# Optimization experiments

Hardware: AMD Instinct MI355X
Metric: run time of the kernel (lower is better)

The kernel has to match this reference:

```python
import jax, jax.numpy as jnp
import numpy as np

N_NODES = 100000
N_EDGES = 1600000
FEATURE_DIM, CONDITION_DIM, HIDDEN_DIM, LATENT_DIM = 256, 64, 128, 64


def setup_inputs() -> dict:
    key = jax.random.key(0)
    ks = jax.random.split(key, 12)

    def glorot(k, fan_in, fan_out):
        s = np.sqrt(6.0 / (fan_in + fan_out)).astype(np.float32)
        return jax.random.uniform(k, (fan_in, fan_out), jnp.float32, -s, s)

    return {
        "feature": jax.random.normal(ks[0], (N_NODES, FEATURE_DIM), jnp.float32),
        "condition": jax.random.normal(ks[1], (N_NODES, CONDITION_DIM), jnp.float32),
        "edge_index": jax.random.randint(ks[2], (2, N_EDGES), 0, N_NODES, jnp.int64),
        "W_f2h": glorot(ks[3], FEATURE_DIM, HIDDEN_DIM),
        "b_f2h": jnp.zeros((HIDDEN_DIM,), jnp.float32),
        "W_c2h": glorot(ks[4], CONDITION_DIM, HIDDEN_DIM),
        "b_c2h": jnp.zeros((HIDDEN_DIM,), jnp.float32),
        "W_h2h": glorot(ks[5], 2 * HIDDEN_DIM, HIDDEN_DIM),
        "b_h2h": jnp.zeros((HIDDEN_DIM,), jnp.float32),
        "W_h2l": glorot(ks[6], HIDDEN_DIM, LATENT_DIM),
        "b_h2l": jnp.zeros((LATENT_DIM,), jnp.float32),
    }


def reference(feature, condition, edge_index, W_f2h, b_f2h, W_c2h, b_c2h,
              W_h2h, b_h2h, W_h2l, b_h2l):
    N = feature.shape[0]
    self_loops = jnp.arange(N, dtype=edge_index.dtype)
    src = jnp.concatenate([edge_index[0], self_loops])  # message sources (j)
    dst = jnp.concatenate([edge_index[1], self_loops])  # message targets (i)

    # symmetric GCN normalization: D^{-1/2} (A+I) D^{-1/2}
    deg = jax.ops.segment_sum(jnp.ones(dst.shape[0], feature.dtype), dst,
                              num_segments=N)
    dinv = jnp.where(deg > 0, jax.lax.rsqrt(deg), 0.0)
    norm = dinv[src] * dinv[dst]  # [E+N]

    def gcn_conv(x, W, b):
        xl = x @ W                                   # [N, out]
        msg = xl[src] * norm[:, None]                # gather + scale
        return jax.ops.segment_sum(msg, dst, num_segments=N) + b

    f2h = jnp.tanh(gcn_conv(feature, W_f2h, b_f2h))
    c2h = jnp.tanh(gcn_conv(condition, W_c2h, b_c2h))
    h = jnp.concatenate([f2h, c2h], axis=1)          # [N, 2*hidden]
    h = jnp.tanh(gcn_conv(h, W_h2h, b_h2h))
    z = gcn_conv(h, W_h2l, b_h2l)
    return z
```

## Files before the change

kernel.cpp:

```cpp
#include <hip/hip_runtime.h>
#include <cmath>
#include <cstdint>


typedef _Float16 f16;
typedef _Float16 f16x8 __attribute__((ext_vector_type(8)));
typedef float f32x4 __attribute__((ext_vector_type(4)));
typedef unsigned int u32x4 __attribute__((ext_vector_type(4)));

__global__ void count_zero_kernel(int* __restrict__ count, int N) {
    int i = blockIdx.x * 256 + threadIdx.x;
    if (i < N) count[i] = 0;
}

__global__ void count_rank_kernel(const int* __restrict__ dst, int* __restrict__ count,
                                  int* __restrict__ rank, int E) {
    int e = blockIdx.x * 256 + threadIdx.x;
    if (e < E) rank[e] = atomicAdd(&count[dst[e]], 1);
}

__global__ void dinv_kernel(const int* __restrict__ count, float* __restrict__ dinv, int N) {
    int i = blockIdx.x * 256 + threadIdx.x;
    if (i < N) dinv[i] = rsqrtf((float)(count[i] + 1));
}

constexpr int SCAN_VPT = 8;
constexpr int SCAN_TILE = 256 * SCAN_VPT;

__global__ __launch_bounds__(256) void scan_partial_kernel(const int* __restrict__ count,
                                                           int* __restrict__ blocksums, int N) {
    __shared__ int red[256];
    const int t = threadIdx.x;
    int base = blockIdx.x * SCAN_TILE + t * SCAN_VPT;
    int s = 0;
#pragma unroll
    for (int i = 0; i < SCAN_VPT; ++i) {
        int idx = base + i;
        if (idx < N) s += count[idx];
    }
    red[t] = s;
    __syncthreads();
    for (int off = 128; off > 0; off >>= 1) {
        if (t < off) red[t] += red[t + off];
        __syncthreads();
    }
    if (t == 0) blocksums[blockIdx.x] = red[0];
}

__global__ __launch_bounds__(1024) void scan_blocksums_kernel(int* __restrict__ blocksums, int nb) {
    __shared__ int sh[1024];
    const int t = threadIdx.x;
    int v = (t < nb) ? blocksums[t] : 0;
    sh[t] = v;
    __syncthreads();
    for (int off = 1; off < 1024; off <<= 1) {
        int u = (t >= off) ? sh[t - off] : 0;
        __syncthreads();
        sh[t] += u;
        __syncthreads();
    }
    if (t < nb) blocksums[t] = sh[t] - v;
}

__global__ __launch_bounds__(256) void scan_final_kernel(const int* __restrict__ count,
                                                         const int* __restrict__ blocksums,
                                                         int* __restrict__ row_ptr, int N) {
    __shared__ int red[256];
    const int t = threadIdx.x;
    int base = blockIdx.x * SCAN_TILE + t * SCAN_VPT;
    int vals[SCAN_VPT];
    int s = 0;
#pragma unroll
    for (int i = 0; i < SCAN_VPT; ++i) {
        int idx = base + i;
        vals[i] = (idx < N) ? count[idx] : 0;
        s += vals[i];
    }
    red[t] = s;
    __syncthreads();
    for (int off = 1; off < 256; off <<= 1) {
        int u = (t >= off) ? red[t - off] : 0;
        __syncthreads();
        red[t] += u;
        __syncthreads();
    }
    int run = red[t] - s + blocksums[blockIdx.x];
#pragma unroll
    for (int i = 0; i < SCAN_VPT; ++i) {
        int idx = base + i;
        if (idx < N) {
            row_ptr[idx] = run;
            run += vals[i];
            if (idx == N - 1) row_ptr[N] = run;
        }
    }
}

__global__ void fill_kernel(const int* __restrict__ src, const int* __restrict__ dst,
                            const int* __restrict__ rank, const float* __restrict__ dinv,
                            const int* __restrict__ row_ptr, long long* __restrict__ csr, int E) {
    int e = blockIdx.x * 256 + threadIdx.x;
    if (e >= E) return;
    int s = src[e];
    int d = dst[e];
    int pos = row_ptr[d] + rank[e];
    float nrm = dinv[s] * dinv[d];
    long long v = ((long long)(unsigned)__float_as_int(nrm) << 32) | (unsigned)s;
    __builtin_nontemporal_store(v, csr + pos);
}

__global__ void wprep_kernel(const float* __restrict__ W, f16* __restrict__ wt_hi,
                             f16* __restrict__ wt_lo, int K, int M) {
    int idx = blockIdx.x * 256 + threadIdx.x;
    if (idx >= K * M) return;
    int k = idx / M, m = idx % M;
    float w = W[idx];
    f16 h = (f16)w;
    wt_hi[(size_t)m * K + k] = h;
    wt_lo[(size_t)m * K + k] = (f16)(w - (float)h);
}

__global__ void f32to16_kernel(const float* __restrict__ x, f16* __restrict__ y, int n4) {
    int i = blockIdx.x * 256 + threadIdx.x;
    if (i < n4) {
        float4 v = ((const float4*)x)[i];
        union { f16 h[4]; uint2 u; } p;
        p.h[0] = (f16)v.x; p.h[1] = (f16)v.y; p.h[2] = (f16)v.z; p.h[3] = (f16)v.w;
        ((uint2*)y)[i] = p.u;
    }
}

template <int K, int M, bool BIAS_TANH, bool X_IS_HALF>
__global__ __launch_bounds__(256) void gemm_mfma_kernel(
    const void* __restrict__ Xv, const f16* __restrict__ Wth,
    const f16* __restrict__ Wtl, const float* __restrict__ bias,
    f16* __restrict__ out, int ld, int colOff, int N) {
    constexpr int BM = 128, BK = 32, XP = 40;
    constexpr int SW = M / 4;
    constexpr int CT = SW / 16;
    constexpr int RT = BM / 16;
    __shared__ f16 xs[BM * XP];
    __shared__ f16 whs[M * XP];
    __shared__ f16 wls[M * XP];

    const int tid = threadIdx.x;
    const int lane = tid & 63;
    const int wv = tid >> 6;
    const int m16 = lane & 15;
    const int quad = lane >> 4;
    const int row0 = blockIdx.x * BM;

    f32x4 acc[RT][CT];
#pragma unroll
    for (int rt = 0; rt < RT; ++rt)
#pragma unroll
        for (int ct = 0; ct < CT; ++ct) acc[rt][ct] = (f32x4){0.f, 0.f, 0.f, 0.f};

    for (int k0 = 0; k0 < K; k0 += BK) {
        if (X_IS_HALF) {
            const f16* X = (const f16*)Xv;
#pragma unroll
            for (int i = 0; i < 2; ++i) {
                int c = i * 256 + tid;
                int r = c >> 2, ko = (c & 3) * 8;
                uint4 v = make_uint4(0u, 0u, 0u, 0u);
                if (row0 + r < N) v = *(const uint4*)(X + (size_t)(row0 + r) * K + k0 + ko);
                *(uint4*)(&xs[r * XP + ko]) = v;
            }
        } else {
            const float* X = (const float*)Xv;
#pragma unroll
            for (int i = 0; i < 4; ++i) {
                int c = i * 256 + tid;
                int r = c >> 3, kq = (c & 7) * 4;
                float4 v = make_float4(0.f, 0.f, 0.f, 0.f);
                if (row0 + r < N) v = *(const float4*)(X + (size_t)(row0 + r) * K + k0 + kq);
                union { f16 h[4]; uint2 u; } p;
                p.h[0] = (f16)v.x; p.h[1] = (f16)v.y; p.h[2] = (f16)v.z; p.h[3] = (f16)v.w;
                *(uint2*)(&xs[r * XP + kq]) = p.u;
            }
        }
#pragma unroll
        for (int i = 0; i < (M * 4) / 256; ++i) {
            int c = i * 256 + tid;
            int n = c >> 2, ko = (c & 3) * 8;
            *(uint4*)(&whs[n * XP + ko]) = *(const uint4*)(Wth + (size_t)n * K + k0 + ko);
            *(uint4*)(&wls[n * XP + ko]) = *(const uint4*)(Wtl + (size_t)n * K + k0 + ko);
        }
        __syncthreads();

        f16x8 bh[CT], bl[CT];
#pragma unroll
        for (int ct = 0; ct < CT; ++ct) {
            bh[ct] = *(const f16x8*)(&whs[(wv * SW + ct * 16 + m16) * XP + quad * 8]);
            bl[ct] = *(const f16x8*)(&wls[(wv * SW + ct * 16 + m16) * XP + quad * 8]);
        }
#pragma unroll
        for (int rt = 0; rt < RT; ++rt) {
            f16x8 a = *(const f16x8*)(&xs[(rt * 16 + m16) * XP + quad * 8]);
#pragma unroll
            for (int ct = 0; ct < CT; ++ct) {
                acc[rt][ct] = __builtin_amdgcn_mfma_f32_16x16x32_f16(a, bh[ct], acc[rt][ct], 0, 0, 0);
                acc[rt][ct] = __builtin_amdgcn_mfma_f32_16x16x32_f16(a, bl[ct], acc[rt][ct], 0, 0, 0);
            }
        }
        __syncthreads();
    }

    float brs[CT];
    if (BIAS_TANH) {
#pragma unroll
        for (int ct = 0; ct < CT; ++ct) brs[ct] = bias[wv * SW + ct * 16 + m16];
    }

#pragma unroll
    for (int rt = 0; rt < RT; ++rt) {
#pragma unroll
        for (int r = 0; r < 4; ++r) {
            int row = row0 + rt * 16 + quad * 4 + r;
            if (row < N) {
                f16* op = out + (size_t)row * ld + colOff + wv * SW + m16;
#pragma unroll
                for (int ct = 0; ct < CT; ++ct) {
                    float v = acc[rt][ct][r];
                    if (BIAS_TANH) v = tanhf(v + brs[ct]);
                    op[ct * 16] = (f16)v;
                }
            }
        }
    }
}

template <int M, bool TANH, bool HAS_BIAS, bool OUT_F32>
__global__ __launch_bounds__(256) void gather_h_kernel(
    const f16* __restrict__ xl, const float* __restrict__ b,
    const float* __restrict__ dinv, const int* __restrict__ row_ptr,
    const int2* __restrict__ csr, void* __restrict__ outv,
    int ld, int colOff, int N) {
    constexpr int TPN = M / 8;
    int gid = blockIdx.x * 256 + threadIdx.x;
    int node = gid / TPN;
    int t = gid % TPN;
    if (node >= N) return;

    float di = dinv[node];
    float self = di * di;
    f16x8 x = *(const f16x8*)(xl + (size_t)node * M + t * 8);
    float acc[8];
#pragma unroll
    for (int j = 0; j < 8; ++j) acc[j] = (float)x[j] * self;
    if (HAS_BIAS) {
        float4 b0 = *(const float4*)(b + t * 8);
        float4 b1 = *(const float4*)(b + t * 8 + 4);
        acc[0] += b0.x; acc[1] += b0.y; acc[2] += b0.z; acc[3] += b0.w;
        acc[4] += b1.x; acc[5] += b1.y; acc[6] += b1.z; acc[7] += b1.w;
    }

    int p = row_ptr[node];
    const int p1 = row_ptr[node + 1];
    for (; p + 4 <= p1; p += 4) {
        int2 e0 = csr[p];
        int2 e1 = csr[p + 1];
        int2 e2 = csr[p + 2];
        int2 e3 = csr[p + 3];
        f16x8 v0 = *(const f16x8*)(xl + (size_t)e0.x * M + t * 8);
        f16x8 v1 = *(const f16x8*)(xl + (size_t)e1.x * M + t * 8);
        f16x8 v2 = *(const f16x8*)(xl + (size_t)e2.x * M + t * 8);
        f16x8 v3 = *(const f16x8*)(xl + (size_t)e3.x * M + t * 8);
        float n0 = __int_as_float(e0.y);
        float n1 = __int_as_float(e1.y);
        float n2 = __int_as_float(e2.y);
        float n3 = __int_as_float(e3.y);
#pragma unroll
        for (int j = 0; j < 8; ++j)
            acc[j] += ((float)v0[j] * n0 + (float)v1[j] * n1) +
                      ((float)v2[j] * n2 + (float)v3[j] * n3);
    }
    for (; p < p1; ++p) {
        int2 e0 = csr[p];
        f16x8 v0 = *(const f16x8*)(xl + (size_t)e0.x * M + t * 8);
        float n0 = __int_as_float(e0.y);
#pragma unroll
        for (int j = 0; j < 8; ++j) acc[j] += (float)v0[j] * n0;
    }

    if (TANH) {
#pragma unroll
        for (int j = 0; j < 8; ++j) acc[j] = tanhf(acc[j]);
    }

    if (OUT_F32) {
        float* op = (float*)outv + (size_t)node * ld + colOff + t * 8;
        f32x4 o0 = {acc[0], acc[1], acc[2], acc[3]};
        f32x4 o1 = {acc[4], acc[5], acc[6], acc[7]};
        __builtin_nontemporal_store(o0, (f32x4*)op);
        __builtin_nontemporal_store(o1, (f32x4*)(op + 4));
    } else {
        union { f16 h[8]; u32x4 u; } o;
#pragma unroll
        for (int j = 0; j < 8; ++j) o.h[j] = (f16)acc[j];
        __builtin_nontemporal_store(o.u, (u32x4*)((f16*)outv + (size_t)node * ld + colOff + t * 8));
    }
}

extern "C" void kernel_launch(void* const* d_in, const int* in_sizes, int n_in,
                              void* d_out, int out_size, void* d_ws, size_t ws_size,
                              hipStream_t stream) {
    const int FD = 256;

    const float* feature   = (const float*)d_in[0];
    const float* condition = (const float*)d_in[1];
    const int*   edge      = (const int*)d_in[2];
    const float* W_f2h = (const float*)d_in[3];
    const float* b_f2h = (const float*)d_in[4];
    const float* W_c2h = (const float*)d_in[5];
    const float* b_c2h = (const float*)d_in[6];
    const float* W_h2h = (const float*)d_in[7];
    const float* b_h2h = (const float*)d_in[8];
    const float* W_h2l = (const float*)d_in[9];
    const float* b_h2l = (const float*)d_in[10];
    float* out = (float*)d_out;

    const int N = in_sizes[0] / FD;
    const int E = in_sizes[2] / 2;
    const int* src = edge;
    const int* dst = edge + E;

    float* ws_f   = (float*)d_ws;
    float* dinv   = ws_f;
    int*   count  = (int*)(ws_f + N);
    int*   rowp   = count + N;
    int*   bsums  = rowp + N + 1;
    int*   rank   = bsums + 1024;
    long long* csr = (long long*)(((uintptr_t)(rank + E) + 15) & ~(uintptr_t)15);
    f16*   A_h    = (f16*)(csr + E);
    f16*   B_h    = A_h + (size_t)N * 128;
    f16*   cond_h = B_h + (size_t)N * 256;
    f16*   wt1h   = cond_h + (size_t)N * 64;
    f16*   wt1l   = wt1h + 128 * 256;
    f16*   wt2h   = wt1l + 128 * 256;
    f16*   wt2l   = wt2h + 128 * 64;
    f16*   wt3h   = wt2l + 128 * 64;
    f16*   wt3l   = wt3h + 128 * 256;
    f16*   wt4h   = wt3l + 128 * 256;
    f16*   wt4l   = wt4h + 64 * 128;

    const int TB = 256;
    dim3 blk(TB);
    const int nScanBlocks = (N + SCAN_TILE - 1) / SCAN_TILE;

    wprep_kernel<<<(256 * 128 + TB - 1) / TB, blk, 0, stream>>>(W_f2h, wt1h, wt1l, 256, 128);
    wprep_kernel<<<(64 * 128 + TB - 1) / TB, blk, 0, stream>>>(W_c2h, wt2h, wt2l, 64, 128);
    wprep_kernel<<<(256 * 128 + TB - 1) / TB, blk, 0, stream>>>(W_h2h, wt3h, wt3l, 256, 128);
    wprep_kernel<<<(128 * 64 + TB - 1) / TB, blk, 0, stream>>>(W_h2l, wt4h, wt4l, 128, 64);
    f32to16_kernel<<<(N * 16 + TB - 1) / TB, blk, 0, stream>>>(condition, cond_h, N * 16);

    count_zero_kernel<<<(N + TB - 1) / TB, blk, 0, stream>>>(count, N);
    count_rank_kernel<<<(E + TB - 1) / TB, blk, 0, stream>>>(dst, count, rank, E);
    dinv_kernel<<<(N + TB - 1) / TB, blk, 0, stream>>>(count, dinv, N);
    scan_partial_kernel<<<nScanBlocks, blk, 0, stream>>>(count, bsums, N);
    scan_blocksums_kernel<<<1, 1024, 0, stream>>>(bsums, nScanBlocks);
    scan_final_kernel<<<nScanBlocks, blk, 0, stream>>>(count, bsums, rowp, N);
    fill_kernel<<<(E + TB - 1) / TB, blk, 0, stream>>>(src, dst, rank, dinv, rowp, csr, E);

    const int gemm_grid = (N + 127) / 128;
    const int g128 = (N * 16 + TB - 1) / TB;
    const int g64  = (N * 8 + TB - 1) / TB;

    gemm_mfma_kernel<256, 128, false, false><<<gemm_grid, blk, 0, stream>>>(
        feature, wt1h, wt1l, nullptr, A_h, 128, 0, N);
    gather_h_kernel<128, true, true, false><<<g128, blk, 0, stream>>>(
        A_h, b_f2h, dinv, rowp, (const int2*)csr, B_h, 256, 0, N);

    gather_h_kernel<64, false, false, false><<<g64, blk, 0, stream>>>(
        cond_h, nullptr, dinv, rowp, (const int2*)csr, A_h, 64, 0, N);
    gemm_mfma_kernel<64, 128, true, true><<<gemm_grid, blk, 0, stream>>>(
        A_h, wt2h, wt2l, b_c2h, B_h, 256, 128, N);

    gemm_mfma_kernel<256, 128, false, true><<<gemm_grid, blk, 0, stream>>>(
        B_h, wt3h, wt3l, nullptr, A_h, 128, 0, N);
    gather_h_kernel<128, true, true, false><<<g128, blk, 0, stream>>>(
        A_h, b_h2h, dinv, rowp, (const int2*)csr, B_h, 128, 0, N);

    gemm_mfma_kernel<128, 64, false, true><<<gemm_grid, blk, 0, stream>>>(
        B_h, wt4h, wt4l, nullptr, A_h, 64, 0, N);
    gather_h_kernel<64, false, true, true><<<g64, blk, 0, stream>>>(
        A_h, b_h2l, dinv, rowp, (const int2*)csr, out, 64, 0, N);
}
```

Baseline: 738.1 us.

## Fuse feature and condition gathers over interleaved XL buffer; prefetch CSR edges

The first GEMM output and the fp16 condition are written side by side in one 192-wide row buffer, so a single fused gather kernel aggregates both over the graph in one CSR pass. This removes a separate gather launch and a second read of the CSR structure. The gather loops now software-prefetch the next four CSR entries with nontemporal loads and handle the tail by masking instead of a scalar remainder loop. The cost is wider strided rows per gathered node, partly padded loads in the masked tail, and an extra ldx parameter on the GEMM.

```diff
diff --git a/kernel.cpp b/kernel.cpp
--- a/kernel.cpp
+++ b/kernel.cpp
@@ -5,8 +5,10 @@
 
 typedef _Float16 f16;
 typedef _Float16 f16x8 __attribute__((ext_vector_type(8)));
+typedef _Float16 f16x4 __attribute__((ext_vector_type(4)));
 typedef float f32x4 __attribute__((ext_vector_type(4)));
 typedef unsigned int u32x4 __attribute__((ext_vector_type(4)));
+typedef unsigned int u32x2 __attribute__((ext_vector_type(2)));
 
 __global__ void count_zero_kernel(int* __restrict__ count, int N) {
     int i = blockIdx.x * 256 + threadIdx.x;
@@ -120,21 +122,21 @@
     wt_lo[(size_t)m * K + k] = (f16)(w - (float)h);
 }
 
-__global__ void f32to16_kernel(const float* __restrict__ x, f16* __restrict__ y, int n4) {
+__global__ void cond_to_xl_kernel(const float* __restrict__ x, f16* __restrict__ XL, int N) {
     int i = blockIdx.x * 256 + threadIdx.x;
-    if (i < n4) {
-        float4 v = ((const float4*)x)[i];
-        union { f16 h[4]; uint2 u; } p;
-        p.h[0] = (f16)v.x; p.h[1] = (f16)v.y; p.h[2] = (f16)v.z; p.h[3] = (f16)v.w;
-        ((uint2*)y)[i] = p.u;
-    }
+    if (i >= N * 16) return;
+    int node = i >> 4, q = i & 15;
+    float4 v = ((const float4*)x)[i];
+    union { f16 h[4]; uint2 u; } p;
+    p.h[0] = (f16)v.x; p.h[1] = (f16)v.y; p.h[2] = (f16)v.z; p.h[3] = (f16)v.w;
+    *(uint2*)(XL + (size_t)node * 192 + 128 + q * 4) = p.u;
 }
 
 template <int K, int M, bool BIAS_TANH, bool X_IS_HALF>
 __global__ __launch_bounds__(256) void gemm_mfma_kernel(
     const void* __restrict__ Xv, const f16* __restrict__ Wth,
     const f16* __restrict__ Wtl, const float* __restrict__ bias,
-    f16* __restrict__ out, int ld, int colOff, int N) {
+    f16* __restrict__ out, int ld, int colOff, int ldx, int N) {
     constexpr int BM = 128, BK = 32, XP = 40;
     constexpr int SW = M / 4;
     constexpr int CT = SW / 16;
@@ -164,7 +166,7 @@
                 int c = i * 256 + tid;
                 int r = c >> 2, ko = (c & 3) * 8;
                 uint4 v = make_uint4(0u, 0u, 0u, 0u);
-                if (row0 + r < N) v = *(const uint4*)(X + (size_t)(row0 + r) * K + k0 + ko);
+                if (row0 + r < N) v = *(const uint4*)(X + (size_t)(row0 + r) * ldx + k0 + ko);
                 *(uint4*)(&xs[r * XP + ko]) = v;
             }
         } else {
@@ -174,7 +176,7 @@
                 int c = i * 256 + tid;
                 int r = c >> 3, kq = (c & 7) * 4;
                 float4 v = make_float4(0.f, 0.f, 0.f, 0.f);
-                if (row0 + r < N) v = *(const float4*)(X + (size_t)(row0 + r) * K + k0 + kq);
+                if (row0 + r < N) v = *(const float4*)(X + (size_t)(row0 + r) * ldx + k0 + kq);
                 union { f16 h[4]; uint2 u; } p;
                 p.h[0] = (f16)v.x; p.h[1] = (f16)v.y; p.h[2] = (f16)v.z; p.h[3] = (f16)v.w;
                 *(uint2*)(&xs[r * XP + kq]) = p.u;
@@ -235,7 +237,7 @@
 __global__ __launch_bounds__(256) void gather_h_kernel(
     const f16* __restrict__ xl, const float* __restrict__ b,
     const float* __restrict__ dinv, const int* __restrict__ row_ptr,
-    const int2* __restrict__ csr, void* __restrict__ outv,
+    const long long* __restrict__ csr, void* __restrict__ outv,
     int ld, int colOff, int N) {
     constexpr int TPN = M / 8;
     int gid = blockIdx.x * 256 + threadIdx.x;
@@ -258,30 +260,37 @@
 
     int p = row_ptr[node];
     const int p1 = row_ptr[node + 1];
-    for (; p + 4 <= p1; p += 4) {
-        int2 e0 = csr[p];
-        int2 e1 = csr[p + 1];
-        int2 e2 = csr[p + 2];
-        int2 e3 = csr[p + 3];
-        f16x8 v0 = *(const f16x8*)(xl + (size_t)e0.x * M + t * 8);
-        f16x8 v1 = *(const f16x8*)(xl + (size_t)e1.x * M + t * 8);
-        f16x8 v2 = *(const f16x8*)(xl + (size_t)e2.x * M + t * 8);
-        f16x8 v3 = *(const f16x8*)(xl + (size_t)e3.x * M + t * 8);
-        float n0 = __int_as_float(e0.y);
-        float n1 = __int_as_float(e1.y);
-        float n2 = __int_as_float(e2.y);
-        float n3 = __int_as_float(e3.y);
+    const int last = p1 - 1;
+    long long e0 = 0, e1 = 0, e2 = 0, e3 = 0;
+    if (p < p1) {
+        e0 = __builtin_nontemporal_load(csr + p);
+        e1 = __builtin_nontemporal_load(csr + (p + 1 < p1 ? p + 1 : last));
+        e2 = __builtin_nontemporal_load(csr + (p + 2 < p1 ? p + 2 : last));
+        e3 = __builtin_nontemporal_load(csr + (p + 3 < p1 ? p + 3 : last));
+    }
+    while (p < p1) {
+        const long long c0 = e0, c1 = e1, c2 = e2, c3 = e3;
+        const int pn = p + 4;
+        if (pn < p1) {
+            e0 = __builtin_nontemporal_load(csr + pn);
+            e1 = __builtin_nontemporal_load(csr + (pn + 1 < p1 ? pn + 1 : last));
+            e2 = __builtin_nontemporal_load(csr + (pn + 2 < p1 ? pn + 2 : last));
+            e3 = __builtin_nontemporal_load(csr + (pn + 3 < p1 ? pn + 3 : last));
+        }
+        int s0 = (int)c0, s1 = (int)c1, s2 = (int)c2, s3 = (int)c3;
+        float n0 = __int_as_float((int)(c0 >> 32));
+        float n1 = (p + 1 < p1) ? __int_as_float((int)(c1 >> 32)) : 0.f;
+        float n2 = (p + 2 < p1) ? __int_as_float((int)(c2 >> 32)) : 0.f;
+        float n3 = (p + 3 < p1) ? __int_as_float((int)(c3 >> 32)) : 0.f;
+        f16x8 v0 = *(const f16x8*)(xl + (size_t)s0 * M + t * 8);
+        f16x8 v1 = *(const f16x8*)(xl + (size_t)s1 * M + t * 8);
+        f16x8 v2 = *(const f16x8*)(xl + (size_t)s2 * M + t * 8);
+        f16x8 v3 = *(const f16x8*)(xl + (size_t)s3 * M + t * 8);
 #pragma unroll
         for (int j = 0; j < 8; ++j)
             acc[j] += ((float)v0[j] * n0 + (float)v1[j] * n1) +
                       ((float)v2[j] * n2 + (float)v3[j] * n3);
-    }
-    for (; p < p1; ++p) {
-        int2 e0 = csr[p];
-        f16x8 v0 = *(const f16x8*)(xl + (size_t)e0.x * M + t * 8);
-        float n0 = __int_as_float(e0.y);
-#pragma unroll
-        for (int j = 0; j < 8; ++j) acc[j] += (float)v0[j] * n0;
+        p = pn;
     }
 
     if (TANH) {
@@ -301,6 +310,92 @@
         for (int j = 0; j < 8; ++j) o.h[j] = (f16)acc[j];
         __builtin_nontemporal_store(o.u, (u32x4*)((f16*)outv + (size_t)node * ld + colOff + t * 8));
     }
+}
+
+__global__ __launch_bounds__(256) void gather_fused_kernel(
+    const f16* __restrict__ XL, const float* __restrict__ bA,
+    const float* __restrict__ dinv, const int* __restrict__ row_ptr,
+    const long long* __restrict__ csr, f16* __restrict__ out, int N) {
+    int gid = blockIdx.x * 256 + threadIdx.x;
+    int node = gid >> 4;
+    int t = gid & 15;
+    if (node >= N) return;
+
+    float di = dinv[node];
+    float self = di * di;
+    const f16* base = XL + (size_t)node * 192;
+    f16x8 xa = *(const f16x8*)(base + t * 8);
+    f16x4 xc = *(const f16x4*)(base + 128 + t * 4);
+    float accA[8], accC[4];
+#pragma unroll
+    for (int j = 0; j < 8; ++j) accA[j] = (float)xa[j] * self;
+#pragma unroll
+    for (int j = 0; j < 4; ++j) accC[j] = (float)xc[j] * self;
+    {
+        float4 b0 = *(const float4*)(bA + t * 8);
+        float4 b1 = *(const float4*)(bA + t * 8 + 4);
+        accA[0] += b0.x; accA[1] += b0.y; accA[2] += b0.z; accA[3] += b0.w;
+        accA[4] += b1.x; accA[5] += b1.y; accA[6] += b1.z; accA[7] += b1.w;
+    }
+
+    int p = row_ptr[node];
+    const int p1 = row_ptr[node + 1];
+    const int last = p1 - 1;
+    long long e0 = 0, e1 = 0, e2 = 0, e3 = 0;
+    if (p < p1) {
+        e0 = __builtin_nontemporal_load(csr + p);
+        e1 = __builtin_nontemporal_load(csr + (p + 1 < p1 ? p + 1 : last));
+        e2 = __builtin_nontemporal_load(csr + (p + 2 < p1 ? p + 2 : last));
+        e3 = __builtin_nontemporal_load(csr + (p + 3 < p1 ? p + 3 : last));
+    }
+    while (p < p1) {
+        const long long c0 = e0, c1 = e1, c2 = e2, c3 = e3;
+        const int pn = p + 4;
+        if (pn < p1) {
+            e0 = __builtin_nontemporal_load(csr + pn);
+            e1 = __builtin_nontemporal_load(csr + (pn + 1 < p1 ? pn + 1 : last));
+            e2 = __builtin_nontemporal_load(csr + (pn + 2 < p1 ? pn + 2 : last));
+            e3 = __builtin_nontemporal_load(csr + (pn + 3 < p1 ? pn + 3 : last));
+        }
+        int s0 = (int)c0, s1 = (int)c1, s2 = (int)c2, s3 = (int)c3;
+        float n0 = __int_as_float((int)(c0 >> 32));
+        float n1 = (p + 1 < p1) ? __int_as_float((int)(c1 >> 32)) : 0.f;
+        float n2 = (p + 2 < p1) ? __int_as_float((int)(c2 >> 32)) : 0.f;
+        float n3 = (p + 3 < p1) ? __int_as_float((int)(c3 >> 32)) : 0.f;
+        const f16* r0 = XL + (size_t)s0 * 192;
+        const f16* r1 = XL + (size_t)s1 * 192;
+        const f16* r2 = XL + (size_t)s2 * 192;
+        const f16* r3 = XL + (size_t)s3 * 192;
+        f16x8 a0 = *(const f16x8*)(r0 + t * 8);
+        f16x8 a1 = *(const f16x8*)(r1 + t * 8);
+        f16x8 a2 = *(const f16x8*)(r2 + t * 8);
+        f16x8 a3 = *(const f16x8*)(r3 + t * 8);
+        f16x4 q0 = *(const f16x4*)(r0 + 128 + t * 4);
+        f16x4 q1 = *(const f16x4*)(r1 + 128 + t * 4);
+        f16x4 q2 = *(const f16x4*)(r2 + 128 + t * 4);
+        f16x4 q3 = *(const f16x4*)(r3 + 128 + t * 4);
+#pragma unroll
+        for (int j = 0; j < 8; ++j)
+            accA[j] += ((float)a0[j] * n0 + (float)a1[j] * n1) +
+                       ((float)a2[j] * n2 + (float)a3[j] * n3);
+#pragma unroll
+        for (int j = 0; j < 4; ++j)
+            accC[j] += ((float)q0[j] * n0 + (float)q1[j] * n1) +
+                       ((float)q2[j] * n2 + (float)q3[j] * n3);
+        p = pn;
+    }
+
+#pragma unroll
+    for (int j = 0; j < 8; ++j) accA[j] = tanhf(accA[j]);
+
+    union { f16 h[8]; u32x4 u; } oa;
+#pragma unroll
+    for (int j = 0; j < 8; ++j) oa.h[j] = (f16)accA[j];
+    __builtin_nontemporal_store(oa.u, (u32x4*)(out + (size_t)node * 256 + t * 8));
+    union { f16 h[4]; u32x2 u; } oc;
+#pragma unroll
+    for (int j = 0; j < 4; ++j) oc.h[j] = (f16)accC[j];
+    __builtin_nontemporal_store(oc.u, (u32x2*)(out + (size_t)node * 256 + 128 + t * 4));
 }
 
 extern "C" void kernel_launch(void* const* d_in, const int* in_sizes, int n_in,
@@ -333,10 +428,9 @@
     int*   bsums  = rowp + N + 1;
     int*   rank   = bsums + 1024;
     long long* csr = (long long*)(((uintptr_t)(rank + E) + 15) & ~(uintptr_t)15);
-    f16*   A_h    = (f16*)(csr + E);
-    f16*   B_h    = A_h + (size_t)N * 128;
-    f16*   cond_h = B_h + (size_t)N * 256;
-    f16*   wt1h   = cond_h + (size_t)N * 64;
+    f16*   XL     = (f16*)(csr + E);
+    f16*   B_h    = XL + (size_t)N * 192;
+    f16*   wt1h   = B_h + (size_t)N * 256;
     f16*   wt1l   = wt1h + 128 * 256;
     f16*   wt2h   = wt1l + 128 * 256;
     f16*   wt2l   = wt2h + 128 * 64;
@@ -353,7 +447,7 @@
     wprep_kernel<<<(64 * 128 + TB - 1) / TB, blk, 0, stream>>>(W_c2h, wt2h, wt2l, 64, 128);
     wprep_kernel<<<(256 * 128 + TB - 1) / TB, blk, 0, stream>>>(W_h2h, wt3h, wt3l, 256, 128);
     wprep_kernel<<<(128 * 64 + TB - 1) / TB, blk, 0, stream>>>(W_h2l, wt4h, wt4l, 128, 64);
-    f32to16_kernel<<<(N * 16 + TB - 1) / TB, blk, 0, stream>>>(condition, cond_h, N * 16);
+    cond_to_xl_kernel<<<(N * 16 + TB - 1) / TB, blk, 0, stream>>>(condition, XL, N);
 
     count_zero_kernel<<<(N + TB - 1) / TB, blk, 0, stream>>>(count, N);
     count_rank_kernel<<<(E + TB - 1) / TB, blk, 0, stream>>>(dst, count, rank, E);
@@ -368,22 +462,21 @@
     const int g64  = (N * 8 + TB - 1) / TB;
 
     gemm_mfma_kernel<256, 128, false, false><<<gemm_grid, blk, 0, stream>>>(
-        feature, wt1h, wt1l, nullptr, A_h, 128, 0, N);
+        feature, wt1h, wt1l, nullptr, XL, 192, 0, 256, N);
+
+    gather_fused_kernel<<<g128, blk, 0, stream>>>(
+        XL, b_f2h, dinv, rowp, csr, B_h, N);
+
+    gemm_mfma_kernel<64, 128, true, true><<<gemm_grid, blk, 0, stream>>>(
+        (const void*)(B_h + 128), wt2h, wt2l, b_c2h, B_h, 256, 128, 256, N);
+
+    gemm_mfma_kernel<256, 128, false, true><<<gemm_grid, blk, 0, stream>>>(
+        B_h, wt3h, wt3l, nullptr, XL, 128, 0, 256, N);
     gather_h_kernel<128, true, true, false><<<g128, blk, 0, stream>>>(
-        A_h, b_f2h, dinv, rowp, (const int2*)csr, B_h, 256, 0, N);
-
-    gather_h_kernel<64, false, false, false><<<g64, blk, 0, stream>>>(
-        cond_h, nullptr, dinv, rowp, (const int2*)csr, A_h, 64, 0, N);
-    gemm_mfma_kernel<64, 128, true, true><<<gemm_grid, blk, 0, stream>>>(
-        A_h, wt2h, wt2l, b_c2h, B_h, 256, 128, N);
-
-    gemm_mfma_kernel<256, 128, false, true><<<gemm_grid, blk, 0, stream>>>(
-        B_h, wt3h, wt3l, nullptr, A_h, 128, 0, N);
-    gather_h_kernel<128, true, true, false><<<g128, blk, 0, stream>>>(
-        A_h, b_h2h, dinv, rowp, (const int2*)csr, B_h, 128, 0, N);
+        XL, b_h2h, dinv, rowp, csr, B_h, 128, 0, N);
 
     gemm_mfma_kernel<128, 64, false, true><<<gemm_grid, blk, 0, stream>>>(
-        B_h, wt4h, wt4l, nullptr, A_h, 64, 0, N);
+        B_h, wt4h, wt4l, nullptr, XL, 64, 0, 128, N);
     gather_h_kernel<64, false, true, true><<<g64, blk, 0, stream>>>(
-        A_h, b_h2l, dinv, rowp, (const int2*)csr, out, 64, 0, N);
-}
+        XL, b_h2l, dinv, rowp, csr, out, 64, 0, N);
+}
```

After: 740.6 us. No clear change (+0.3%).
